# Performance work log

Hardware: AMD Instinct MI355X
Metric: run time of the kernel (lower is better)

## Reference

```python
import jax, jax.numpy as jnp
import numpy as np

DIM_MODEL = 1024
DIM_LLM = 4096
HEAD_NUM = 16
DIM_KEYS = DIM_MODEL // HEAD_NUM  # 64


def setup_inputs() -> dict:
    key = jax.random.key(0)
    ks = jax.random.split(key, 11)
    B, P, V = 8, 256, 8192
    s_q = 1.0 / np.sqrt(DIM_MODEL)
    s_l = 1.0 / np.sqrt(DIM_LLM)
    s_d = 1.0 / np.sqrt(DIM_MODEL)
    return {
        "query": jax.random.normal(ks[0], (B, P, DIM_MODEL), dtype=jnp.float32),
        "key": jax.random.normal(ks[1], (V, DIM_LLM), dtype=jnp.float32),
        "value": jax.random.normal(ks[2], (V, DIM_LLM), dtype=jnp.float32),
        "Wq": jax.random.normal(ks[3], (DIM_MODEL, DIM_MODEL), dtype=jnp.float32) * s_q,
        "bq": jnp.zeros((DIM_MODEL,), dtype=jnp.float32),
        "Wk": jax.random.normal(ks[4], (DIM_LLM, DIM_MODEL), dtype=jnp.float32) * s_l,
        "bk": jnp.zeros((DIM_MODEL,), dtype=jnp.float32),
        "Wv": jax.random.normal(ks[5], (DIM_LLM, DIM_MODEL), dtype=jnp.float32) * s_l,
        "bv": jnp.zeros((DIM_MODEL,), dtype=jnp.float32),
        "Wo": jax.random.normal(ks[6], (DIM_MODEL, DIM_LLM), dtype=jnp.float32) * s_d,
        "bo": jnp.zeros((DIM_LLM,), dtype=jnp.float32),
    }


def reference(query, key, value, Wq, bq, Wk, bk, Wv, bv, Wo, bo):
    B, P, _ = query.shape
    V = key.shape[0]
    # projections
    q = (query @ Wq + bq).reshape(B, P, HEAD_NUM, DIM_KEYS)        # [b,p,h,k]
    k = (key @ Wk + bk).reshape(V, HEAD_NUM, DIM_KEYS)             # [v,h,k]
    v = (value @ Wv + bv).reshape(V, HEAD_NUM, DIM_KEYS)           # [v,h,k]
    scale = 1.0 / DIM_KEYS  # NOTE: original uses 1/d_k, not 1/sqrt(d_k)
    scores = jnp.einsum('bphk,vhk->bhpv', q, k)                    # [b,h,p,v]
    A = jax.nn.softmax(scale * scores, axis=-1)                    # dropout is identity in eval
    mapped = jnp.einsum('bhpv,vhk->bphk', A, v)                    # [b,p,h,k]
    mapped = mapped.reshape(B, P, HEAD_NUM * DIM_KEYS)
    return mapped @ Wo + bo                                        # [b,p,dim_llm]
```

## Files before the change

### kernel.cpp

```cpp
#include <hip/hip_runtime.h>


typedef __attribute__((ext_vector_type(8)))  short          short8;
typedef __attribute__((ext_vector_type(4)))  float          f32x4;
typedef __attribute__((ext_vector_type(16))) float          f32x16;
typedef __attribute__((ext_vector_type(8)))  unsigned short ushort8;
typedef __attribute__((ext_vector_type(2)))  unsigned int   uint2v;

__device__ __forceinline__ unsigned short f2bf(float f) {
    unsigned int u = __builtin_bit_cast(unsigned int, f);
    u += 0x7fffu + ((u >> 16) & 1u);
    return (unsigned short)(u >> 16);
}

__device__ __forceinline__ void gld_lds16(const ushort* g, ushort* l) {
    __builtin_amdgcn_global_load_lds(
        (const __attribute__((address_space(1))) void*)g,
        (__attribute__((address_space(3))) void*)l, 16, 0, 0);
}

__global__ __launch_bounds__(256) void conv_f32_bf16(
    const float* __restrict__ in, ushort* __restrict__ out, int n)
{
    int i = (blockIdx.x * 256 + threadIdx.x) * 8;
    if (i >= n) return;
    float4 a = *(const float4*)(in + i);
    float4 b = *(const float4*)(in + i + 4);
    ushort8 o = {f2bf(a.x), f2bf(a.y), f2bf(a.z), f2bf(a.w),
                 f2bf(b.x), f2bf(b.y), f2bf(b.z), f2bf(b.w)};
    *(ushort8*)(out + i) = o;
}

__global__ __launch_bounds__(256) void transconv(
    const float* __restrict__ in, ushort* __restrict__ out, int R, int C)
{
    __shared__ float t[32][33];
    const int tx = threadIdx.x & 31, ty = threadIdx.x >> 5;
    const int bx = blockIdx.x, by = blockIdx.y;
#pragma unroll
    for (int i = 0; i < 4; ++i)
        t[ty + 8 * i][tx] = in[(size_t)(by * 32 + ty + 8 * i) * C + bx * 32 + tx];
    __syncthreads();
#pragma unroll
    for (int i = 0; i < 4; ++i)
        out[(size_t)(bx * 32 + ty + 8 * i) * R + by * 32 + tx] = f2bf(t[tx][ty + 8 * i]);
}

template<int OUT_BF16, int BIAS_ROW>
__global__ __launch_bounds__(256) void gemm_bt(
    const ushort* __restrict__ A, const ushort* __restrict__ BT,
    const float* __restrict__ bias, void* __restrict__ Cout,
    int M, int N, int K, float oscale)
{
    __shared__ ushort As[128 * 32];
    __shared__ ushort Bs[128 * 32];
    const int tid = threadIdx.x;
    const int w = tid >> 6, lane = tid & 63;
    const int m = lane & 15, quad = lane >> 4;
    const int wr = w >> 1, wc = w & 1;
    const int bx = blockIdx.x, by = blockIdx.y;

    f32x4 acc[4][4];
#pragma unroll
    for (int i = 0; i < 4; ++i)
#pragma unroll
        for (int j = 0; j < 4; ++j)
#pragma unroll
            for (int r = 0; r < 4; ++r) acc[i][j][r] = 0.f;

    const int r_i = lane >> 2;
    const int ccl = (lane & 3) ^ ((lane >> 2) & 3) ^ quad;
    const ushort* Ag = A  + (size_t)(by * 128 + w * 32 + r_i) * K + ccl * 8;
    const ushort* Bg = BT + (size_t)(bx * 128 + w * 32 + r_i) * K + ccl * 8;
    ushort* AsW = As + w * 1024;
    ushort* BsW = Bs + w * 1024;
    const size_t rowstep = (size_t)16 * K;

    const int phys = (quad ^ (m & 3) ^ (m >> 2)) * 8;
    int aoff[4], boff[4];
#pragma unroll
    for (int i = 0; i < 4; ++i) {
        aoff[i] = (wr * 64 + i * 16 + m) * 32 + phys;
        boff[i] = (wc * 64 + i * 16 + m) * 32 + phys;
    }

    const int kIters = K >> 5;
    for (int kt = 0; kt < kIters; ++kt) {
        __syncthreads();
        gld_lds16(Ag, AsW);
        gld_lds16(Ag + rowstep, AsW + 512);
        gld_lds16(Bg, BsW);
        gld_lds16(Bg + rowstep, BsW + 512);
        Ag += 32; Bg += 32;
        __syncthreads();
        short8 af[4], bf[4];
#pragma unroll
        for (int i = 0; i < 4; ++i) af[i] = *(const short8*)(As + aoff[i]);
#pragma unroll
        for (int i = 0; i < 4; ++i) bf[i] = *(const short8*)(Bs + boff[i]);
#pragma unroll
        for (int i = 0; i < 4; ++i)
#pragma unroll
            for (int j = 0; j < 4; ++j)
                acc[i][j] = __builtin_amdgcn_mfma_f32_16x16x32_bf16(
                    af[i], bf[j], acc[i][j], 0, 0, 0);
    }

    const int row0 = by * 128 + wr * 64;
    const int col0 = bx * 128 + wc * 64;
#pragma unroll
    for (int i = 0; i < 4; ++i) {
#pragma unroll
        for (int j = 0; j < 4; ++j) {
            const int c = col0 + j * 16 + m;
            float bcol = BIAS_ROW ? 0.f : bias[c];
#pragma unroll
            for (int r = 0; r < 4; ++r) {
                const int rw = row0 + i * 16 + quad * 4 + r;
                float v = acc[i][j][r] + (BIAS_ROW ? bias[rw] : bcol);
                v *= oscale;
                if (OUT_BF16)
                    ((ushort*)Cout)[(size_t)rw * N + c] = f2bf(v);
                else
                    ((float*)Cout)[(size_t)rw * N + c] = v;
            }
        }
    }
}

__global__ __launch_bounds__(256, 2) void attn_mfma(
    const ushort* __restrict__ qb, const ushort* __restrict__ kb,
    const ushort* __restrict__ vT, ushort* __restrict__ mappedb)
{
    __shared__ ushort Qs[64 * 64];
    __shared__ ushort Ks[128 * 64];
    __shared__ ushort Vs[64 * 128];
    __shared__ short  Ps[64 * 136];

    const int tid = threadIdx.x;
    const int w = tid >> 6, lane = tid & 63;
    const int l31 = lane & 31, l5 = lane >> 5, quad = lane >> 4;
    const int wp = w >> 1, wv = w & 1;
    const int idx = blockIdx.x;
    const int pt = idx & 3, h = (idx >> 2) & 15, b = idx >> 6;
    const int pbase = b * 256 + pt * 64;

    const int c8 = lane & 7, r8 = lane >> 3, c16 = lane & 15;

#pragma unroll
    for (int j = 0; j < 2; ++j) {
        const int t = w * 2 + j;
        const ushort* g = qb + (size_t)(pbase + t * 8 + r8) * 1024 + h * 64 + c8 * 8;
        gld_lds16(g, Qs + t * 512);
    }
    __syncthreads();
    short8 qf[4];
#pragma unroll
    for (int ks = 0; ks < 4; ++ks)
        qf[ks] = *(const short8*)(Qs + (wp * 32 + l31) * 64 + ks * 16 + l5 * 8);

    f32x16 o[2];
#pragma unroll
    for (int dt = 0; dt < 2; ++dt)
#pragma unroll
        for (int r = 0; r < 16; ++r) o[dt][r] = 0.f;
    float lpart = 0.f;

    const int ccK = c8 ^ r8;
    const int prow = (wp * 32 + l31) * 136;

    for (int vt = 0; vt < 8192; vt += 128) {
        __syncthreads();
#pragma unroll
        for (int i = 0; i < 4; ++i) {
            const int t = w * 4 + i;
            const ushort* gk = kb + (size_t)(vt + t * 8 + r8) * 1024 + h * 64 + ccK * 8;
            gld_lds16(gk, Ks + t * 512);
            const int d_l = t * 4 + quad;
            const int ccV = c16 ^ (d_l & 15);
            const ushort* gv = vT + (size_t)(h * 64 + d_l) * 8192 + vt + ccV * 8;
            gld_lds16(gv, Vs + t * 512);
        }
        __syncthreads();

        f32x16 st[2];
#pragma unroll
        for (int s = 0; s < 2; ++s)
#pragma unroll
            for (int r = 0; r < 16; ++r) st[s][r] = 0.f;
        __builtin_amdgcn_s_setprio(1);
#pragma unroll
        for (int s = 0; s < 2; ++s) {
            const int v4 = wv * 2 + s;
            const int row = (v4 * 32 + l31) * 64;
            const int sw = l31 & 7;
#pragma unroll
            for (int ks = 0; ks < 4; ++ks) {
                const int ph = ((ks * 2 + l5) ^ sw) * 8;
                short8 kf = *(const short8*)(Ks + row + ph);
                st[s] = __builtin_amdgcn_mfma_f32_32x32x16_bf16(kf, qf[ks], st[s], 0, 0, 0);
            }
        }
        __builtin_amdgcn_s_setprio(0);

#pragma unroll
        for (int s = 0; s < 2; ++s) {
            const int v4 = wv * 2 + s;
#pragma unroll
            for (int g = 0; g < 4; ++g) {
                float e0 = exp2f(st[s][g * 4 + 0]);
                float e1 = exp2f(st[s][g * 4 + 1]);
                float e2 = exp2f(st[s][g * 4 + 2]);
                float e3 = exp2f(st[s][g * 4 + 3]);
                lpart += (e0 + e1) + (e2 + e3);
                unsigned int plo, phi;
                asm("v_cvt_pk_bf16_f32 %0, %1, %2" : "=v"(plo) : "v"(e0), "v"(e1));
                asm("v_cvt_pk_bf16_f32 %0, %1, %2" : "=v"(phi) : "v"(e2), "v"(e3));
                uint2v pk = {plo, phi};
                *(uint2v*)(Ps + prow + v4 * 32 + g * 8 + l5 * 4) = pk;
            }
        }
        asm volatile("s_waitcnt lgkmcnt(0)" ::: "memory");
        __builtin_amdgcn_sched_barrier(0);

        __builtin_amdgcn_s_setprio(1);
#pragma unroll
        for (int k4 = 0; k4 < 4; ++k4) {
            const int k8 = wv * 4 + k4;
            short8 pf = *(const short8*)(Ps + prow + k8 * 16 + l5 * 8);
#pragma unroll
            for (int dt = 0; dt < 2; ++dt) {
                const int d_l = dt * 32 + l31;
                const int ph = ((k8 * 2 + l5) ^ (d_l & 15)) * 8;
                short8 vf = *(const short8*)(Vs + d_l * 128 + ph);
                o[dt] = __builtin_amdgcn_mfma_f32_32x32x16_bf16(pf, vf, o[dt], 0, 0, 0);
            }
        }
        __builtin_amdgcn_s_setprio(0);
    }

    __syncthreads();
    float* Red  = (float*)Ks;
    float* Lred = (float*)Vs;
    if (wv == 1) {
#pragma unroll
        for (int dt = 0; dt < 2; ++dt)
#pragma unroll
            for (int r = 0; r < 16; ++r)
                Red[wp * 2048 + (dt * 16 + r) * 64 + lane] = o[dt][r];
        Lred[wp * 64 + lane] = lpart;
    }
    __syncthreads();
    if (wv == 0) {
#pragma unroll
        for (int dt = 0; dt < 2; ++dt)
#pragma unroll
            for (int r = 0; r < 16; ++r)
                o[dt][r] += Red[wp * 2048 + (dt * 16 + r) * 64 + lane];
        lpart += Lred[wp * 64 + lane];

        float lfull = lpart + __shfl_xor(lpart, 32, 64);
        float rinv = 1.0f / lfull;
#pragma unroll
        for (int r = 0; r < 16; ++r) {
            const int poff = (r & 3) + 8 * (r >> 2) + 4 * l5;
            const float sc = __shfl(rinv, poff, 64);
            const size_t grow = (size_t)(pbase + wp * 32 + poff) * 1024;
#pragma unroll
            for (int dt = 0; dt < 2; ++dt)
                mappedb[grow + h * 64 + dt * 32 + l31] = f2bf(o[dt][r] * sc);
        }
    }
}

extern "C" void kernel_launch(void* const* d_in, const int* in_sizes, int n_in,
                              void* d_out, int out_size, void* d_ws, size_t ws_size,
                              hipStream_t stream)
{
    const float* query = (const float*)d_in[0];
    const float* key   = (const float*)d_in[1];
    const float* value = (const float*)d_in[2];
    const float* Wq    = (const float*)d_in[3];
    const float* bq    = (const float*)d_in[4];
    const float* Wk    = (const float*)d_in[5];
    const float* bk    = (const float*)d_in[6];
    const float* Wv    = (const float*)d_in[7];
    const float* bv    = (const float*)d_in[8];
    const float* Wo    = (const float*)d_in[9];
    const float* bo    = (const float*)d_in[10];
    float* out = (float*)d_out;

    char* ws = (char*)d_ws;
    ushort* tmpb    = (ushort*)ws;
    ushort* wslot   = (ushort*)(ws + (64ull << 20));
    ushort* queryb  = (ushort*)(ws + (72ull << 20));
    ushort* qb      = (ushort*)(ws + (76ull << 20));
    ushort* mappedb = (ushort*)ws;
    ushort* kb      = (ushort*)d_out;
    ushort* vT      = (ushort*)((char*)d_out + (16ull << 20));

    const float QSCALE = 1.4426950408889634f / 64.0f;

    conv_f32_bf16<<<16384, 256, 0, stream>>>(key, tmpb, 8192 * 4096);
    transconv<<<dim3(32, 128), 256, 0, stream>>>(Wk, wslot, 4096, 1024);
    gemm_bt<1, 0><<<dim3(8, 64), 256, 0, stream>>>(tmpb, wslot, bk, kb,
                                                   8192, 1024, 4096, 1.0f);
    conv_f32_bf16<<<16384, 256, 0, stream>>>(value, tmpb, 8192 * 4096);
    transconv<<<dim3(32, 128), 256, 0, stream>>>(Wv, wslot, 4096, 1024);
    gemm_bt<1, 1><<<dim3(64, 8), 256, 0, stream>>>(wslot, tmpb, bv, vT,
                                                   1024, 8192, 4096, 1.0f);
    conv_f32_bf16<<<1024, 256, 0, stream>>>(query, queryb, 2048 * 1024);
    transconv<<<dim3(32, 32), 256, 0, stream>>>(Wq, wslot, 1024, 1024);
    gemm_bt<1, 0><<<dim3(8, 16), 256, 0, stream>>>(queryb, wslot, bq, qb,
                                                   2048, 1024, 1024, QSCALE);
    attn_mfma<<<512, 256, 0, stream>>>(qb, kb, vT, mappedb);
    transconv<<<dim3(128, 32), 256, 0, stream>>>(Wo, wslot, 1024, 4096);
    gemm_bt<0, 0><<<dim3(32, 16), 256, 0, stream>>>(mappedb, wslot, bo, out,
                                                    2048, 4096, 1024, 1.0f);
}
```

Measured before the change: 722.7 us.

## Keep softmax probabilities in registers via permlane swap and use 8 waves

The attention kernel stops staging the exponentiated scores through an LDS buffer. It repacks them into MFMA A-operand layout with v_permlane32_swap, so the PV matmul consumes them straight from registers. The block grows from 4 to 8 waves, each handling one 32-column slice of the V tile, which adds a two-stage cross-wave reduction of the output accumulators at the end. This removes the LDS write/read round trip and its waitcnt stall per tile, at the cost of more reduction traffic and a different occupancy target (launch bounds 512,4).

```diff
diff --git a/kernel.cpp b/kernel.cpp
--- a/kernel.cpp
+++ b/kernel.cpp
@@ -5,7 +5,7 @@
 typedef __attribute__((ext_vector_type(4)))  float          f32x4;
 typedef __attribute__((ext_vector_type(16))) float          f32x16;
 typedef __attribute__((ext_vector_type(8)))  unsigned short ushort8;
-typedef __attribute__((ext_vector_type(2)))  unsigned int   uint2v;
+typedef __attribute__((ext_vector_type(4)))  unsigned int   uint4v;
 
 __device__ __forceinline__ unsigned short f2bf(float f) {
     unsigned int u = __builtin_bit_cast(unsigned int, f);
@@ -128,30 +128,27 @@
     }
 }
 
-__global__ __launch_bounds__(256, 2) void attn_mfma(
+__global__ __launch_bounds__(512, 4) void attn_mfma(
     const ushort* __restrict__ qb, const ushort* __restrict__ kb,
     const ushort* __restrict__ vT, ushort* __restrict__ mappedb)
 {
     __shared__ ushort Qs[64 * 64];
     __shared__ ushort Ks[128 * 64];
     __shared__ ushort Vs[64 * 128];
-    __shared__ short  Ps[64 * 136];
 
     const int tid = threadIdx.x;
     const int w = tid >> 6, lane = tid & 63;
     const int l31 = lane & 31, l5 = lane >> 5, quad = lane >> 4;
-    const int wp = w >> 1, wv = w & 1;
+    const int wp = w >> 2, wv = w & 3;
     const int idx = blockIdx.x;
     const int pt = idx & 3, h = (idx >> 2) & 15, b = idx >> 6;
     const int pbase = b * 256 + pt * 64;
 
     const int c8 = lane & 7, r8 = lane >> 3, c16 = lane & 15;
 
-#pragma unroll
-    for (int j = 0; j < 2; ++j) {
-        const int t = w * 2 + j;
-        const ushort* g = qb + (size_t)(pbase + t * 8 + r8) * 1024 + h * 64 + c8 * 8;
-        gld_lds16(g, Qs + t * 512);
+    {
+        const ushort* g = qb + (size_t)(pbase + w * 8 + r8) * 1024 + h * 64 + c8 * 8;
+        gld_lds16(g, Qs + w * 512);
     }
     __syncthreads();
     short8 qf[4];
@@ -167,13 +164,12 @@
     float lpart = 0.f;
 
     const int ccK = c8 ^ r8;
-    const int prow = (wp * 32 + l31) * 136;
 
     for (int vt = 0; vt < 8192; vt += 128) {
         __syncthreads();
 #pragma unroll
-        for (int i = 0; i < 4; ++i) {
-            const int t = w * 4 + i;
+        for (int i = 0; i < 2; ++i) {
+            const int t = w * 2 + i;
             const ushort* gk = kb + (size_t)(vt + t * 8 + r8) * 1024 + h * 64 + ccK * 8;
             gld_lds16(gk, Ks + t * 512);
             const int d_l = t * 4 + quad;
@@ -183,51 +179,39 @@
         }
         __syncthreads();
 
-        f32x16 st[2];
-#pragma unroll
-        for (int s = 0; s < 2; ++s)
-#pragma unroll
-            for (int r = 0; r < 16; ++r) st[s][r] = 0.f;
-        __builtin_amdgcn_s_setprio(1);
-#pragma unroll
-        for (int s = 0; s < 2; ++s) {
-            const int v4 = wv * 2 + s;
-            const int row = (v4 * 32 + l31) * 64;
+        f32x16 st;
+#pragma unroll
+        for (int r = 0; r < 16; ++r) st[r] = 0.f;
+        {
+            const int row = (wv * 32 + l31) * 64;
             const int sw = l31 & 7;
+            __builtin_amdgcn_s_setprio(1);
 #pragma unroll
             for (int ks = 0; ks < 4; ++ks) {
                 const int ph = ((ks * 2 + l5) ^ sw) * 8;
                 short8 kf = *(const short8*)(Ks + row + ph);
-                st[s] = __builtin_amdgcn_mfma_f32_32x32x16_bf16(kf, qf[ks], st[s], 0, 0, 0);
+                st = __builtin_amdgcn_mfma_f32_32x32x16_bf16(kf, qf[ks], st, 0, 0, 0);
             }
-        }
-        __builtin_amdgcn_s_setprio(0);
-
-#pragma unroll
-        for (int s = 0; s < 2; ++s) {
-            const int v4 = wv * 2 + s;
-#pragma unroll
-            for (int g = 0; g < 4; ++g) {
-                float e0 = exp2f(st[s][g * 4 + 0]);
-                float e1 = exp2f(st[s][g * 4 + 1]);
-                float e2 = exp2f(st[s][g * 4 + 2]);
-                float e3 = exp2f(st[s][g * 4 + 3]);
-                lpart += (e0 + e1) + (e2 + e3);
-                unsigned int plo, phi;
-                asm("v_cvt_pk_bf16_f32 %0, %1, %2" : "=v"(plo) : "v"(e0), "v"(e1));
-                asm("v_cvt_pk_bf16_f32 %0, %1, %2" : "=v"(phi) : "v"(e2), "v"(e3));
-                uint2v pk = {plo, phi};
-                *(uint2v*)(Ps + prow + v4 * 32 + g * 8 + l5 * 4) = pk;
-            }
-        }
-        asm volatile("s_waitcnt lgkmcnt(0)" ::: "memory");
-        __builtin_amdgcn_sched_barrier(0);
-
-        __builtin_amdgcn_s_setprio(1);
-#pragma unroll
-        for (int k4 = 0; k4 < 4; ++k4) {
-            const int k8 = wv * 4 + k4;
-            short8 pf = *(const short8*)(Ps + prow + k8 * 16 + l5 * 8);
+            __builtin_amdgcn_s_setprio(0);
+        }
+
+#pragma unroll
+        for (int k4 = 0; k4 < 2; ++k4) {
+            float e[8];
+#pragma unroll
+            for (int t = 0; t < 8; ++t) e[t] = exp2f(st[k4 * 8 + t]);
+            lpart += ((e[0] + e[1]) + (e[2] + e[3])) + ((e[4] + e[5]) + (e[6] + e[7]));
+            unsigned int a0, a1, b0, b1;
+            asm("v_cvt_pk_bf16_f32 %0, %1, %2" : "=v"(a0) : "v"(e[0]), "v"(e[1]));
+            asm("v_cvt_pk_bf16_f32 %0, %1, %2" : "=v"(a1) : "v"(e[2]), "v"(e[3]));
+            asm("v_cvt_pk_bf16_f32 %0, %1, %2" : "=v"(b0) : "v"(e[4]), "v"(e[5]));
+            asm("v_cvt_pk_bf16_f32 %0, %1, %2" : "=v"(b1) : "v"(e[6]), "v"(e[7]));
+            asm("v_permlane32_swap_b32 %0, %1" : "+v"(a0), "+v"(b0));
+            asm("v_permlane32_swap_b32 %0, %1" : "+v"(a1), "+v"(b1));
+            uint4v pfw = {a0, a1, b0, b1};
+            short8 pf = __builtin_bit_cast(short8, pfw);
+            const int k8 = wv * 2 + k4;
+            __builtin_amdgcn_s_setprio(1);
 #pragma unroll
             for (int dt = 0; dt < 2; ++dt) {
                 const int d_l = dt * 32 + l31;
@@ -235,20 +219,39 @@
                 short8 vf = *(const short8*)(Vs + d_l * 128 + ph);
                 o[dt] = __builtin_amdgcn_mfma_f32_32x32x16_bf16(pf, vf, o[dt], 0, 0, 0);
             }
-        }
-        __builtin_amdgcn_s_setprio(0);
-    }
-
-    __syncthreads();
-    float* Red  = (float*)Ks;
-    float* Lred = (float*)Vs;
+            __builtin_amdgcn_s_setprio(0);
+        }
+    }
+
+    float* RedA = (float*)Ks;
+    float* RedB = (float*)Vs;
+    float* Lq   = (float*)Qs;
+    Lq[w * 64 + lane] = lpart;
+    __syncthreads();
+    if (wv >= 2) {
+        float* R = (wv == 2) ? RedA : RedB;
+#pragma unroll
+        for (int dt = 0; dt < 2; ++dt)
+#pragma unroll
+            for (int r = 0; r < 16; ++r)
+                R[wp * 2048 + (dt * 16 + r) * 64 + lane] = o[dt][r];
+    }
+    __syncthreads();
+    if (wv < 2) {
+        float* R = (wv == 0) ? RedA : RedB;
+#pragma unroll
+        for (int dt = 0; dt < 2; ++dt)
+#pragma unroll
+            for (int r = 0; r < 16; ++r)
+                o[dt][r] += R[wp * 2048 + (dt * 16 + r) * 64 + lane];
+    }
+    __syncthreads();
     if (wv == 1) {
 #pragma unroll
         for (int dt = 0; dt < 2; ++dt)
 #pragma unroll
             for (int r = 0; r < 16; ++r)
-                Red[wp * 2048 + (dt * 16 + r) * 64 + lane] = o[dt][r];
-        Lred[wp * 64 + lane] = lpart;
+                RedA[wp * 2048 + (dt * 16 + r) * 64 + lane] = o[dt][r];
     }
     __syncthreads();
     if (wv == 0) {
@@ -256,10 +259,11 @@
         for (int dt = 0; dt < 2; ++dt)
 #pragma unroll
             for (int r = 0; r < 16; ++r)
-                o[dt][r] += Red[wp * 2048 + (dt * 16 + r) * 64 + lane];
-        lpart += Lred[wp * 64 + lane];
-
-        float lfull = lpart + __shfl_xor(lpart, 32, 64);
+                o[dt][r] += RedA[wp * 2048 + (dt * 16 + r) * 64 + lane];
+        float lsum = (Lq[(wp * 4 + 0) * 64 + lane] + Lq[(wp * 4 + 1) * 64 + lane])
+                   + (Lq[(wp * 4 + 2) * 64 + lane] + Lq[(wp * 4 + 3) * 64 + lane]);
+
+        float lfull = lsum + __shfl_xor(lsum, 32, 64);
         float rinv = 1.0f / lfull;
 #pragma unroll
         for (int r = 0; r < 16; ++r) {
@@ -313,7 +317,7 @@
     transconv<<<dim3(32, 32), 256, 0, stream>>>(Wq, wslot, 1024, 1024);
     gemm_bt<1, 0><<<dim3(8, 16), 256, 0, stream>>>(queryb, wslot, bq, qb,
                                                    2048, 1024, 1024, QSCALE);
-    attn_mfma<<<512, 256, 0, stream>>>(qb, kb, vT, mappedb);
+    attn_mfma<<<512, 512, 0, stream>>>(qb, kb, vT, mappedb);
     transconv<<<dim3(128, 32), 256, 0, stream>>>(Wo, wslot, 1024, 4096);
     gemm_bt<0, 0><<<dim3(32, 16), 256, 0, stream>>>(mappedb, wslot, bo, out,
                                                     2048, 4096, 1024, 1.0f);
```

Result: no change. 713.0 us (-1.3%).
